# Optimization experiments

Hardware: AMD Instinct MI355X
Metric: run time of the kernel (lower is better)

## Reference

```python
import jax, jax.numpy as jnp
import numpy as np

NUM_CLASSES = 10
P_CUTOFF = 0.95
TEMP = 0.5  # temperature used throughout the original forward
B_LB, B_ULB, D = 4096, 6144, 128


def _l2_normalize(x, eps=1e-12):
    # matches torch.nn.functional.normalize(x, dim=1)
    n = jnp.linalg.norm(x, axis=1, keepdims=True)
    return x / jnp.maximum(n, eps)


def setup_inputs() -> dict:
    key = jax.random.key(0)
    k = jax.random.split(key, 6)
    anchor_feat = jax.random.normal(k[0], (B_ULB, D), jnp.float32)
    positive_feat = jax.random.normal(k[1], (B_ULB, D), jnp.float32)
    lb_feat = jax.random.normal(k[2], (B_LB, D), jnp.float32)
    labels = jax.random.randint(k[3], (B_LB,), 0, NUM_CLASSES)
    lb_one_hot = jax.nn.one_hot(labels, NUM_CLASSES, dtype=jnp.float32)
    # scale logits so a realistic fraction of unlabeled samples pass the 0.95 cutoff
    logits_x_ulb_1 = 3.0 * jax.random.normal(k[4], (B_ULB, NUM_CLASSES), jnp.float32)
    logits_x_ulb_2 = 3.0 * jax.random.normal(k[5], (B_ULB, NUM_CLASSES), jnp.float32)
    return {
        "anchor_feat": anchor_feat,
        "positive_feat": positive_feat,
        "lb_feat": lb_feat,
        "lb_one_hot": lb_one_hot,
        "logits_x_ulb_1": logits_x_ulb_1,
        "logits_x_ulb_2": logits_x_ulb_2,
    }


def reference(anchor_feat, positive_feat, lb_feat, lb_one_hot,
              logits_x_ulb_1, logits_x_ulb_2):
    # pick the more-confident view per unlabeled sample
    prob1 = jax.nn.softmax(logits_x_ulb_1 / TEMP, axis=1)
    prob2 = jax.nn.softmax(logits_x_ulb_2 / TEMP, axis=1)
    take1 = jnp.max(prob1, axis=-1) >= jnp.max(prob2, axis=-1)
    logits_gt = jnp.where(take1[:, None], logits_x_ulb_1, logits_x_ulb_2)

    # confidence mask at p_cutoff = 0.95
    mask = (jax.nn.softmax(logits_gt, axis=1) >= P_CUTOFF).astype(logits_gt.dtype)
    logits_gt = logits_gt * mask

    # per-class counts: labeled via one-hot sum; unlabeled via vectorized bincount
    class_num_lb = lb_one_hot.sum(axis=0)
    max_val = jnp.max(logits_gt, axis=1)
    max_idx = jnp.argmax(logits_gt, axis=1)
    valid = (max_val != 0).astype(jnp.float32)  # max_val==0 -> idx -1 -> skipped
    class_num_ulb = jnp.zeros((NUM_CLASSES,), jnp.float32).at[max_idx].add(valid) * 2.0
    class_num = class_num_ulb + class_num_lb

    # build [B_lb + 2*B_ulb, 10] target distribution
    logits_x_ulb = jnp.concatenate([logits_gt, logits_gt], axis=0)
    prob_xulb = jax.nn.softmax(logits_x_ulb / TEMP, axis=-1)
    logits_bf = jnp.concatenate([lb_one_hot, prob_xulb], axis=0)  # [N, 10]

    # self-attention over normalized features (second normalize in the original
    # is idempotent on already unit-norm rows)
    feats = _l2_normalize(jnp.concatenate([lb_feat, anchor_feat, positive_feat], axis=0))  # [N, D]
    attn = jax.nn.softmax(feats @ feats.T / TEMP, axis=1)  # [N, N]
    self_atten = attn @ logits_bf  # [N, 10]

    # per-class division; zero-count classes divided by total count
    denom = jnp.where(class_num == 0, class_num.sum(), class_num)
    logits_af = self_atten / denom[None, :]
    return logits_af
```

## Files before the change

### kernel.cpp

```cpp
#include <hip/hip_runtime.h>
#include <hip/hip_bf16.h>

#define NLB 4096
#define NULB 6144
#define NROWS 16384
#define DD 128
#define NC 10
#define VW 12
#define SEG 16
#define JSEG (NROWS / SEG)
#define NTILE (JSEG / 64)
#define BI 256
#define BJ 64
#define NVB 256
#define SQRTC 1.6986437f

typedef __bf16 bf16_t;
typedef _Float16 f16_t;
typedef f16_t f16x8 __attribute__((ext_vector_type(8)));
typedef float f32x4 __attribute__((ext_vector_type(4)));
typedef short i16x2 __attribute__((ext_vector_type(2)));
typedef int i32x8 __attribute__((ext_vector_type(8)));
typedef unsigned int u32;
typedef unsigned char u8;

__device__ __forceinline__ size_t f8idx(int row, int c) {
  return ((size_t)(row >> 7) << 14) + (size_t)((row & 127) << 7)
       + (size_t)(((c ^ (row & 7)) & 7) << 4);
}

__device__ __forceinline__ u32 packexp2f16(float c0, float c1) {
#if __has_builtin(__builtin_amdgcn_cvt_pknorm_i16)
  float y0 = fmaf(c0, 1.2207465e-4f, 0.46740490f);
  float y1 = fmaf(c1, 1.2207465e-4f, 0.46740490f);
  union { i16x2 p; u32 u; } cv;
  cv.p = __builtin_amdgcn_cvt_pknorm_i16(y0, y1);
  return cv.u;
#else
  u32 b0 = (u32)(int)fmaf(c0, 4.0f, 15315.354f);
  u32 b1 = (u32)(int)fmaf(c1, 4.0f, 15315.354f);
  return __builtin_amdgcn_perm(b1, b0, 0x05040100u);
#endif
}

__global__ void kprep2(const float* __restrict__ lb, const float* __restrict__ an,
                       const float* __restrict__ po, const float* __restrict__ onehot,
                       const float* __restrict__ l1, const float* __restrict__ l2,
                       u8* __restrict__ F8, f16_t* __restrict__ VF,
                       float* __restrict__ clsPart) {
  __shared__ float Vtmp[64 * 16];
  __shared__ float lcnt[NC];
  int b = blockIdx.x;
  int t = threadIdx.x;

  if (b < 1024) {
    int row = b * 16 + (t >> 4);
    int c = t & 15;
    const float* src;
    if (row < NLB) src = lb + (size_t)row * DD;
    else if (row < NLB + NULB) src = an + (size_t)(row - NLB) * DD;
    else src = po + (size_t)(row - NLB - NULB) * DD;
    float4 v0 = ((const float4*)src)[c * 2];
    float4 v1 = ((const float4*)src)[c * 2 + 1];
    float ss = v0.x*v0.x + v0.y*v0.y + v0.z*v0.z + v0.w*v0.w
             + v1.x*v1.x + v1.y*v1.y + v1.z*v1.z + v1.w*v1.w;
#pragma unroll
    for (int off = 8; off >= 1; off >>= 1) ss += __shfl_xor(ss, off);
    float inv = (16.0f * SQRTC) / fmaxf(sqrtf(ss), 1e-12f);
    u32 d0 = (u32)__builtin_amdgcn_cvt_pk_fp8_f32(v0.x*inv, v0.y*inv, 0, false);
    d0 = (u32)__builtin_amdgcn_cvt_pk_fp8_f32(v0.z*inv, v0.w*inv, d0, true);
    u32 d1 = (u32)__builtin_amdgcn_cvt_pk_fp8_f32(v1.x*inv, v1.y*inv, 0, false);
    d1 = (u32)__builtin_amdgcn_cvt_pk_fp8_f32(v1.z*inv, v1.w*inv, d1, true);
    uint2 dd = {d0, d1};
    *(uint2*)(F8 + f8idx(row, c >> 1) + ((c & 1) << 3)) = dd;
    return;
  }

  int vb = b - 1024;
  if (t < NC) lcnt[t] = 0.0f;
  __syncthreads();
  if (t < 64) {
    int gid = vb * 64 + t;
    float p[16];
    p[10] = 1.0f; p[11] = 0.f; p[12] = 0.f; p[13] = 0.f; p[14] = 0.f; p[15] = 0.f;
    if (gid < NLB) {
      int idx = 0;
#pragma unroll
      for (int c = 0; c < NC; ++c) {
        p[c] = onehot[(size_t)gid * NC + c];
        if (p[c] == 1.0f) idx = c;
      }
      atomicAdd(&lcnt[idx], 1.0f);
    } else {
      int r = (gid < NLB + NULB) ? (gid - NLB) : (gid - NLB - NULB);
      bool count = (gid < NLB + NULB);
      float a[NC], bb[NC];
#pragma unroll
      for (int c = 0; c < NC; ++c) { a[c] = l1[(size_t)r * NC + c]; bb[c] = l2[(size_t)r * NC + c]; }
      float m1 = a[0], m2 = bb[0];
#pragma unroll
      for (int c = 1; c < NC; ++c) { m1 = fmaxf(m1, a[c]); m2 = fmaxf(m2, bb[c]); }
      float s1 = 0.0f, s2 = 0.0f;
#pragma unroll
      for (int c = 0; c < NC; ++c) {
        s1 += expf(2.0f * (a[c] - m1));
        s2 += expf(2.0f * (bb[c] - m2));
      }
      bool take1 = (s1 <= s2);
      float g[NC];
#pragma unroll
      for (int c = 0; c < NC; ++c) g[c] = take1 ? a[c] : bb[c];
      float mg = g[0];
#pragma unroll
      for (int c = 1; c < NC; ++c) mg = fmaxf(mg, g[c]);
      float e[NC]; float sg = 0.0f;
#pragma unroll
      for (int c = 0; c < NC; ++c) { e[c] = expf(g[c] - mg); sg += e[c]; }
      float msk[NC];
#pragma unroll
      for (int c = 0; c < NC; ++c) msk[c] = ((e[c] / sg) >= 0.95f) ? g[c] : 0.0f;
      float mx = msk[0]; int mi = 0;
#pragma unroll
      for (int c = 1; c < NC; ++c) if (msk[c] > mx) { mx = msk[c]; mi = c; }
      if (count && mx != 0.0f) atomicAdd(&lcnt[mi], 2.0f);
      float mm = 2.0f * msk[0];
#pragma unroll
      for (int c = 1; c < NC; ++c) mm = fmaxf(mm, 2.0f * msk[c]);
      float q[NC]; float sp = 0.0f;
#pragma unroll
      for (int c = 0; c < NC; ++c) { q[c] = expf(2.0f * msk[c] - mm); sp += q[c]; }
#pragma unroll
      for (int c = 0; c < NC; ++c) p[c] = q[c] / sp;
    }
#pragma unroll
    for (int c = 0; c < 16; ++c) Vtmp[t * 16 + c] = p[c];
  }
  __syncthreads();
  if (t < 16) clsPart[(size_t)vb * 16 + t] = (t < NC) ? lcnt[t] : 0.0f;
  if (t < 128) {
    int gbase = vb * 2;
    int G = t >> 6;
    int l = t & 63;
    int q = l >> 4;
    int n = l & 15;
    union { f16_t h[8]; uint4 uu; } pk;
#pragma unroll
    for (int d = 0; d < 4; ++d) {
      pk.h[d]     = (f16_t)Vtmp[(G * 32      + q * 4 + d) * 16 + n];
      pk.h[4 + d] = (f16_t)Vtmp[(G * 32 + 16 + q * 4 + d) * 16 + n];
    }
    *(uint4*)(VF + ((size_t)(gbase + G) * 64 + l) * 8) = pk.uu;
  }
}

#define WAITV(n) asm volatile("s_waitcnt vmcnt(" #n ")" ::: "memory")
__launch_bounds__(256, 4)
__global__ void kattn(const u8* __restrict__ F8, const f16_t* __restrict__ VF,
                      float* __restrict__ Ppart) {
  __shared__ __align__(16) u8 Fs[3][BJ * 128];
  __shared__ uint4 Vs4[3][128];
  int t = threadIdx.x;
  int lane = t & 63;
  int wave = t >> 6;
  int q = lane >> 4;
  int r = lane & 15;
  int i0 = blockIdx.x * BI + wave * 64;
  int jbase = blockIdx.y * JSEG;

  i32x8 bfr[4];
#pragma unroll
  for (int s = 0; s < 4; ++s) {
    int row = i0 + s * 16 + r;
    union { uint4 h[2]; i32x8 v; } bb;
    bb.h[0] = *(const uint4*)(F8 + f8idx(row, 2 * q));
    bb.h[1] = *(const uint4*)(F8 + f8idx(row, 2 * q + 1));
    bfr[s] = bb.v;
  }

  f32x4 acc[4];
#pragma unroll
  for (int s = 0; s < 4; ++s) acc[s] = (f32x4){0.f, 0.f, 0.f, 0.f};
  const f32x4 kZero = {0.f, 0.f, 0.f, 0.f};

  auto stage = [&](int buf, int j0) {
    const uint4* srcF = (const uint4*)(F8 + (((size_t)(j0 >> 7)) << 14)
                                          + (((size_t)(j0 & 64)) << 7));
#pragma unroll
    for (int k = 0; k < 2; ++k) {
      int off = (k << 8) + t;
      __builtin_amdgcn_global_load_lds(
          (const __attribute__((address_space(1))) uint4*)(srcF + off),
          (__attribute__((address_space(3))) uint4*)((uint4*)Fs[buf] + off), 16, 0, 0);
    }
    int vc = t & 127;
    const uint4* srcV = (const uint4*)VF + ((size_t)(j0 >> 5) << 6);
    __builtin_amdgcn_global_load_lds(
        (const __attribute__((address_space(1))) uint4*)(srcV + vc),
        (__attribute__((address_space(3))) uint4*)(Vs4[buf] + vc), 16, 0, 0);
  };

  auto compute = [&](int buf) {
    const u8* fsb = Fs[buf];
    const uint4* vsb = Vs4[buf];
#pragma unroll
    for (int jp = 0; jp < 2; ++jp) {
      union { uint4 h[2]; i32x8 v; } afe, afo;
      const u8* re = fsb + (jp * 32 + r) * 128;
      const u8* ro = re + 16 * 128;
      int c0 = (((2 * q) ^ (r & 7)) & 7) << 4;
      int c1 = (((2 * q + 1) ^ (r & 7)) & 7) << 4;
      afe.h[0] = *(const uint4*)(re + c0);
      afe.h[1] = *(const uint4*)(re + c1);
      afo.h[0] = *(const uint4*)(ro + c0);
      afo.h[1] = *(const uint4*)(ro + c1);
      union { uint4 qd; f16x8 v; } bv;
      bv.qd = vsb[jp * 64 + lane];

      __builtin_amdgcn_s_setprio(1);
      f32x4 ce = __builtin_amdgcn_mfma_scale_f32_16x16x128_f8f6f4(
          afe.v, bfr[0], kZero, 0, 0, 0, 0x7F7F7F7Fu, 0, 0x7F7F7F7Fu);
      f32x4 co = __builtin_amdgcn_mfma_scale_f32_16x16x128_f8f6f4(
          afo.v, bfr[0], kZero, 0, 0, 0, 0x7F7F7F7Fu, 0, 0x7F7F7F7Fu);
      __builtin_amdgcn_s_setprio(0);
#pragma unroll
      for (int s = 0; s < 4; ++s) {
        f32x4 cen, con;
        if (s < 3) {
          __builtin_amdgcn_s_setprio(1);
          cen = __builtin_amdgcn_mfma_scale_f32_16x16x128_f8f6f4(
              afe.v, bfr[s + 1], kZero, 0, 0, 0, 0x7F7F7F7Fu, 0, 0x7F7F7F7Fu);
          con = __builtin_amdgcn_mfma_scale_f32_16x16x128_f8f6f4(
              afo.v, bfr[s + 1], kZero, 0, 0, 0, 0x7F7F7F7Fu, 0, 0x7F7F7F7Fu);
          __builtin_amdgcn_s_setprio(0);
        }
        union { u32 u[4]; f16x8 v; } pf;
        pf.u[0] = packexp2f16(ce[0], ce[1]);
        pf.u[1] = packexp2f16(ce[2], ce[3]);
        pf.u[2] = packexp2f16(co[0], co[1]);
        pf.u[3] = packexp2f16(co[2], co[3]);
        __builtin_amdgcn_s_setprio(1);
        acc[s] = __builtin_amdgcn_mfma_f32_16x16x32_f16(pf.v, bv.v, acc[s], 0, 0, 0);
        __builtin_amdgcn_s_setprio(0);
        if (s < 3) { ce = cen; co = con; }
      }
    }
  };

  stage(0, jbase);
  stage(1, jbase + BJ);
#pragma unroll
  for (int jt = 0; jt < NTILE; ++jt) {
    if (jt + 2 < NTILE) stage((jt + 2) % 3, jbase + (jt + 2) * BJ);
    if (jt + 2 < NTILE)      { WAITV(6); }
    else if (jt + 1 < NTILE) { WAITV(3); }
    else                     { WAITV(0); }
    __builtin_amdgcn_s_barrier();
    __builtin_amdgcn_sched_barrier(0);
    compute(jt % 3);
    __builtin_amdgcn_sched_barrier(0);
    __builtin_amdgcn_s_barrier();
  }

  if (r < 12) {
    float* base = Ppart + ((size_t)blockIdx.y * NROWS + (size_t)i0) * VW;
#pragma unroll
    for (int s = 0; s < 4; ++s) {
      float* op = base + (s * 16 + q * 4) * VW + r;
      op[0 * VW] = acc[s][0];
      op[1 * VW] = acc[s][1];
      op[2 * VW] = acc[s][2];
      op[3 * VW] = acc[s][3];
    }
  }
}

__global__ void kfinal(float* __restrict__ out, const float* __restrict__ Ppart,
                       const float* __restrict__ clsPart) {
  __shared__ float clsS[16];
  int t = threadIdx.x;
  const float4* cp = (const float4*)clsPart;
  float4 c0 = {0.f, 0.f, 0.f, 0.f}, c1 = c0;
  float c2x = 0.f, c2y = 0.f;
#pragma unroll
  for (int k = 0; k < 4; ++k) {
    int rr = t + 64 * k;
    float4 x0 = cp[rr * 4], x1 = cp[rr * 4 + 1], x2 = cp[rr * 4 + 2];
    c0.x += x0.x; c0.y += x0.y; c0.z += x0.z; c0.w += x0.w;
    c1.x += x1.x; c1.y += x1.y; c1.z += x1.z; c1.w += x1.w;
    c2x += x2.x; c2y += x2.y;
  }
#pragma unroll
  for (int off = 32; off >= 1; off >>= 1) {
    c0.x += __shfl_xor(c0.x, off); c0.y += __shfl_xor(c0.y, off);
    c0.z += __shfl_xor(c0.z, off); c0.w += __shfl_xor(c0.w, off);
    c1.x += __shfl_xor(c1.x, off); c1.y += __shfl_xor(c1.y, off);
    c1.z += __shfl_xor(c1.z, off); c1.w += __shfl_xor(c1.w, off);
    c2x += __shfl_xor(c2x, off); c2y += __shfl_xor(c2y, off);
  }
  if (t == 0) {
    *(float4*)&clsS[0] = c0;
    *(float4*)&clsS[4] = c1;
    clsS[8] = c2x; clsS[9] = c2y;
    clsS[10] = 0.f; clsS[11] = 0.f; clsS[12] = 0.f;
    clsS[13] = 0.f; clsS[14] = 0.f; clsS[15] = 0.f;
  }
  __syncthreads();
  float d[NC]; float tot = 0.0f;
#pragma unroll
  for (int c = 0; c < NC; ++c) { d[c] = clsS[c]; tot += d[c]; }

  int row = blockIdx.x * 64 + t;
  float4 a0 = {0.f, 0.f, 0.f, 0.f}, a1 = a0, a2 = a0;
#pragma unroll
  for (int s = 0; s < SEG; ++s) {
    const float4* pr = (const float4*)(Ppart + ((size_t)s * NROWS + (size_t)row) * VW);
    float4 x0 = pr[0], x1 = pr[1], x2 = pr[2];
    a0.x += x0.x; a0.y += x0.y; a0.z += x0.z; a0.w += x0.w;
    a1.x += x1.x; a1.y += x1.y; a1.z += x1.z; a1.w += x1.w;
    a2.x += x2.x; a2.y += x2.y; a2.z += x2.z;
  }
  float num[NC] = {a0.x, a0.y, a0.z, a0.w, a1.x, a1.y, a1.z, a1.w, a2.x, a2.y};
  float rs = 1.0f / a2.z;
  float* op = out + (size_t)row * NC;
#pragma unroll
  for (int c = 0; c < NC; ++c) {
    float den = (d[c] == 0.0f) ? tot : d[c];
    op[c] = num[c] * rs / den;
  }
}

extern "C" void kernel_launch(void* const* d_in, const int* in_sizes, int n_in,
                              void* d_out, int out_size, void* d_ws, size_t ws_size,
                              hipStream_t stream) {
  const float* anchor   = (const float*)d_in[0];
  const float* positive = (const float*)d_in[1];
  const float* lbfeat   = (const float*)d_in[2];
  const float* onehot   = (const float*)d_in[3];
  const float* l1       = (const float*)d_in[4];
  const float* l2       = (const float*)d_in[5];
  float* out = (float*)d_out;

  char* ws = (char*)d_ws;
  u8*     F8      = (u8*)ws;
  f16_t*  VF      = (f16_t*)(ws + 2097152);
  float*  Ppart   = (float*)(ws + 2097152 + 524288);
  float*  clsPart = (float*)(ws + 2097152 + 524288 + (size_t)SEG * NROWS * VW * 4);

  kprep2<<<1024 + NVB, 256, 0, stream>>>(lbfeat, anchor, positive, onehot, l1, l2,
                                         F8, VF, clsPart);
  kattn<<<dim3(NROWS / BI, SEG), 256, 0, stream>>>(F8, VF, Ppart);
  kfinal<<<NVB, 64, 0, stream>>>(out, Ppart, clsPart);
}
```

Measured before the change: 112.0 us.

## Fuse prep, attention and final reduce into one cooperative kernel with grid syncs

Merges the three launches into a single cooperative kernel of 1024 blocks that runs the prep, attention and reduction phases separated by grid-wide syncs. Prep now handles 16 value rows per block alongside feature quantization, and the final reduction spreads the 16 segment partials across lanes with shuffles. If the cooperative launch fails it falls back to three separate kernels. The aim is to remove inter-kernel launch gaps and tail effects, at the cost of grid-sync overhead and a fixed 1024-block grid that must be co-resident at 4 blocks per CU.

```diff
diff --git a/kernel.cpp b/kernel.cpp
--- a/kernel.cpp
+++ b/kernel.cpp
@@ -1,5 +1,8 @@
 #include <hip/hip_runtime.h>
 #include <hip/hip_bf16.h>
+#include <hip/hip_cooperative_groups.h>
+
+namespace cg = cooperative_groups;
 
 #define NLB 4096
 #define NULB 6144
@@ -12,7 +15,6 @@
 #define NTILE (JSEG / 64)
 #define BI 256
 #define BJ 64
-#define NVB 256
 #define SQRTC 1.6986437f
 
 typedef __bf16 bf16_t;
@@ -43,17 +45,15 @@
 #endif
 }
 
-__global__ void kprep2(const float* __restrict__ lb, const float* __restrict__ an,
-                       const float* __restrict__ po, const float* __restrict__ onehot,
-                       const float* __restrict__ l1, const float* __restrict__ l2,
-                       u8* __restrict__ F8, f16_t* __restrict__ VF,
-                       float* __restrict__ clsPart) {
-  __shared__ float Vtmp[64 * 16];
-  __shared__ float lcnt[NC];
-  int b = blockIdx.x;
-  int t = threadIdx.x;
-
-  if (b < 1024) {
+__device__ __forceinline__ void phaseA(
+    const float* __restrict__ lb, const float* __restrict__ an,
+    const float* __restrict__ po, const float* __restrict__ onehot,
+    const float* __restrict__ l1, const float* __restrict__ l2,
+    u8* __restrict__ F8, f16_t* __restrict__ VF, float* __restrict__ clsPart,
+    int b, int t) {
+  __shared__ float Vtmp[16 * 16];
+  __shared__ float lcnt[16];
+  {
     int row = b * 16 + (t >> 4);
     int c = t & 15;
     const float* src;
@@ -73,14 +73,11 @@
     d1 = (u32)__builtin_amdgcn_cvt_pk_fp8_f32(v1.z*inv, v1.w*inv, d1, true);
     uint2 dd = {d0, d1};
     *(uint2*)(F8 + f8idx(row, c >> 1) + ((c & 1) << 3)) = dd;
-    return;
-  }
-
-  int vb = b - 1024;
-  if (t < NC) lcnt[t] = 0.0f;
+  }
+  if (t < 16) lcnt[t] = 0.0f;
   __syncthreads();
-  if (t < 64) {
-    int gid = vb * 64 + t;
+  if (t < 16) {
+    int gid = b * 16 + t;
     float p[16];
     p[10] = 1.0f; p[11] = 0.f; p[12] = 0.f; p[13] = 0.f; p[14] = 0.f; p[15] = 0.f;
     if (gid < NLB) {
@@ -136,36 +133,29 @@
     for (int c = 0; c < 16; ++c) Vtmp[t * 16 + c] = p[c];
   }
   __syncthreads();
-  if (t < 16) clsPart[(size_t)vb * 16 + t] = (t < NC) ? lcnt[t] : 0.0f;
-  if (t < 128) {
-    int gbase = vb * 2;
-    int G = t >> 6;
-    int l = t & 63;
-    int q = l >> 4;
-    int n = l & 15;
-    union { f16_t h[8]; uint4 uu; } pk;
-#pragma unroll
-    for (int d = 0; d < 4; ++d) {
-      pk.h[d]     = (f16_t)Vtmp[(G * 32      + q * 4 + d) * 16 + n];
-      pk.h[4 + d] = (f16_t)Vtmp[(G * 32 + 16 + q * 4 + d) * 16 + n];
-    }
-    *(uint4*)(VF + ((size_t)(gbase + G) * 64 + l) * 8) = pk.uu;
+  if (t < 16) clsPart[(size_t)b * 16 + t] = (t < NC) ? lcnt[t] : 0.0f;
+  if (t < 64) {
+    int l = t, q = l >> 4, n = l & 15;
+    union { f16_t h[4]; uint2 u; } pk;
+#pragma unroll
+    for (int d = 0; d < 4; ++d) pk.h[d] = (f16_t)Vtmp[(q * 4 + d) * 16 + n];
+    *(uint2*)(VF + ((size_t)(b >> 1) * 64 + l) * 8 + (size_t)(b & 1) * 4) = pk.u;
   }
 }
 
 #define WAITV(n) asm volatile("s_waitcnt vmcnt(" #n ")" ::: "memory")
-__launch_bounds__(256, 4)
-__global__ void kattn(const u8* __restrict__ F8, const f16_t* __restrict__ VF,
-                      float* __restrict__ Ppart) {
+__device__ __forceinline__ void phaseB(const u8* __restrict__ F8,
+                                       const f16_t* __restrict__ VF,
+                                       float* __restrict__ Ppart,
+                                       int bx, int by, int t) {
   __shared__ __align__(16) u8 Fs[3][BJ * 128];
   __shared__ uint4 Vs4[3][128];
-  int t = threadIdx.x;
   int lane = t & 63;
   int wave = t >> 6;
   int q = lane >> 4;
   int r = lane & 15;
-  int i0 = blockIdx.x * BI + wave * 64;
-  int jbase = blockIdx.y * JSEG;
+  int i0 = bx * BI + wave * 64;
+  int jbase = by * JSEG;
 
   i32x8 bfr[4];
 #pragma unroll
@@ -262,7 +252,7 @@
   }
 
   if (r < 12) {
-    float* base = Ppart + ((size_t)blockIdx.y * NROWS + (size_t)i0) * VW;
+    float* base = Ppart + ((size_t)by * NROWS + (size_t)i0) * VW;
 #pragma unroll
     for (int s = 0; s < 4; ++s) {
       float* op = base + (s * 16 + q * 4) * VW + r;
@@ -274,59 +264,84 @@
   }
 }
 
-__global__ void kfinal(float* __restrict__ out, const float* __restrict__ Ppart,
-                       const float* __restrict__ clsPart) {
+__device__ __forceinline__ void phaseC(float* __restrict__ out,
+                                       const float* __restrict__ Ppart,
+                                       const float* __restrict__ clsPart,
+                                       int b, int t) {
+  __shared__ float4 LDSc[4][4];
   __shared__ float clsS[16];
-  int t = threadIdx.x;
   const float4* cp = (const float4*)clsPart;
-  float4 c0 = {0.f, 0.f, 0.f, 0.f}, c1 = c0;
-  float c2x = 0.f, c2y = 0.f;
-#pragma unroll
-  for (int k = 0; k < 4; ++k) {
-    int rr = t + 64 * k;
-    float4 x0 = cp[rr * 4], x1 = cp[rr * 4 + 1], x2 = cp[rr * 4 + 2];
-    c0.x += x0.x; c0.y += x0.y; c0.z += x0.z; c0.w += x0.w;
-    c1.x += x1.x; c1.y += x1.y; c1.z += x1.z; c1.w += x1.w;
-    c2x += x2.x; c2y += x2.y;
-  }
-#pragma unroll
-  for (int off = 32; off >= 1; off >>= 1) {
-    c0.x += __shfl_xor(c0.x, off); c0.y += __shfl_xor(c0.y, off);
-    c0.z += __shfl_xor(c0.z, off); c0.w += __shfl_xor(c0.w, off);
-    c1.x += __shfl_xor(c1.x, off); c1.y += __shfl_xor(c1.y, off);
-    c1.z += __shfl_xor(c1.z, off); c1.w += __shfl_xor(c1.w, off);
-    c2x += __shfl_xor(c2x, off); c2y += __shfl_xor(c2y, off);
-  }
-  if (t == 0) {
-    *(float4*)&clsS[0] = c0;
-    *(float4*)&clsS[4] = c1;
-    clsS[8] = c2x; clsS[9] = c2y;
-    clsS[10] = 0.f; clsS[11] = 0.f; clsS[12] = 0.f;
-    clsS[13] = 0.f; clsS[14] = 0.f; clsS[15] = 0.f;
-  }
+  float4 ca = {0.f, 0.f, 0.f, 0.f};
+#pragma unroll
+  for (int k = 0; k < 16; ++k) {
+    float4 x = cp[t + 256 * k];
+    ca.x += x.x; ca.y += x.y; ca.z += x.z; ca.w += x.w;
+  }
+#pragma unroll
+  for (int off = 4; off <= 32; off <<= 1) {
+    ca.x += __shfl_xor(ca.x, off); ca.y += __shfl_xor(ca.y, off);
+    ca.z += __shfl_xor(ca.z, off); ca.w += __shfl_xor(ca.w, off);
+  }
+  int wv = t >> 6, ln = t & 63;
+  if (ln < 4) LDSc[wv][ln] = ca;
   __syncthreads();
-  float d[NC]; float tot = 0.0f;
-#pragma unroll
-  for (int c = 0; c < NC; ++c) { d[c] = clsS[c]; tot += d[c]; }
-
-  int row = blockIdx.x * 64 + t;
-  float4 a0 = {0.f, 0.f, 0.f, 0.f}, a1 = a0, a2 = a0;
-#pragma unroll
-  for (int s = 0; s < SEG; ++s) {
-    const float4* pr = (const float4*)(Ppart + ((size_t)s * NROWS + (size_t)row) * VW);
-    float4 x0 = pr[0], x1 = pr[1], x2 = pr[2];
-    a0.x += x0.x; a0.y += x0.y; a0.z += x0.z; a0.w += x0.w;
-    a1.x += x1.x; a1.y += x1.y; a1.z += x1.z; a1.w += x1.w;
-    a2.x += x2.x; a2.y += x2.y; a2.z += x2.z;
-  }
-  float num[NC] = {a0.x, a0.y, a0.z, a0.w, a1.x, a1.y, a1.z, a1.w, a2.x, a2.y};
-  float rs = 1.0f / a2.z;
-  float* op = out + (size_t)row * NC;
-#pragma unroll
-  for (int c = 0; c < NC; ++c) {
-    float den = (d[c] == 0.0f) ? tot : d[c];
-    op[c] = num[c] * rs / den;
-  }
+  if (t < 4) {
+    float4 s0 = LDSc[0][t], s1 = LDSc[1][t], s2 = LDSc[2][t], s3 = LDSc[3][t];
+    float4 s = {s0.x + s1.x + s2.x + s3.x, s0.y + s1.y + s2.y + s3.y,
+                s0.z + s1.z + s2.z + s3.z, s0.w + s1.w + s2.w + s3.w};
+    *(float4*)&clsS[t * 4] = s;
+  }
+  __syncthreads();
+
+  int row = b * 16 + (t >> 4);
+  int s = t & 15;
+  const float4* pr = (const float4*)(Ppart + ((size_t)s * NROWS + (size_t)row) * VW);
+  float4 a0 = pr[0], a1 = pr[1], a2 = pr[2];
+#pragma unroll
+  for (int off = 1; off <= 8; off <<= 1) {
+    a0.x += __shfl_xor(a0.x, off); a0.y += __shfl_xor(a0.y, off);
+    a0.z += __shfl_xor(a0.z, off); a0.w += __shfl_xor(a0.w, off);
+    a1.x += __shfl_xor(a1.x, off); a1.y += __shfl_xor(a1.y, off);
+    a1.z += __shfl_xor(a1.z, off); a1.w += __shfl_xor(a1.w, off);
+    a2.x += __shfl_xor(a2.x, off); a2.y += __shfl_xor(a2.y, off);
+    a2.z += __shfl_xor(a2.z, off);
+  }
+  if (s < NC) {
+    float num = (s == 0) ? a0.x : (s == 1) ? a0.y : (s == 2) ? a0.z : (s == 3) ? a0.w
+              : (s == 4) ? a1.x : (s == 5) ? a1.y : (s == 6) ? a1.z : (s == 7) ? a1.w
+              : (s == 8) ? a2.x : a2.y;
+    float d = clsS[s];
+    float tot = clsS[0] + clsS[1] + clsS[2] + clsS[3] + clsS[4]
+              + clsS[5] + clsS[6] + clsS[7] + clsS[8] + clsS[9];
+    float den = (d == 0.0f) ? tot : d;
+    float rs = 1.0f / a2.z;
+    out[(size_t)row * NC + s] = num * rs / den;
+  }
+}
+
+__launch_bounds__(256, 4)
+__global__ void kfused(const float* lb, const float* an, const float* po,
+                       const float* onehot, const float* l1, const float* l2,
+                       u8* F8, f16_t* VF, float* clsPart, float* Ppart, float* out) {
+  int b = blockIdx.x, t = threadIdx.x;
+  phaseA(lb, an, po, onehot, l1, l2, F8, VF, clsPart, b, t);
+  cg::this_grid().sync();
+  phaseB(F8, VF, Ppart, b & 63, b >> 6, t);
+  cg::this_grid().sync();
+  phaseC(out, Ppart, clsPart, b, t);
+}
+
+__global__ void kA(const float* lb, const float* an, const float* po,
+                   const float* onehot, const float* l1, const float* l2,
+                   u8* F8, f16_t* VF, float* clsPart) {
+  phaseA(lb, an, po, onehot, l1, l2, F8, VF, clsPart, blockIdx.x, threadIdx.x);
+}
+__launch_bounds__(256, 4)
+__global__ void kB(const u8* F8, const f16_t* VF, float* Ppart) {
+  phaseB(F8, VF, Ppart, blockIdx.x, blockIdx.y, threadIdx.x);
+}
+__global__ void kC(float* out, const float* Ppart, const float* clsPart) {
+  phaseC(out, Ppart, clsPart, blockIdx.x, threadIdx.x);
 }
 
 extern "C" void kernel_launch(void* const* d_in, const int* in_sizes, int n_in,
@@ -346,8 +361,15 @@
   float*  Ppart   = (float*)(ws + 2097152 + 524288);
   float*  clsPart = (float*)(ws + 2097152 + 524288 + (size_t)SEG * NROWS * VW * 4);
 
-  kprep2<<<1024 + NVB, 256, 0, stream>>>(lbfeat, anchor, positive, onehot, l1, l2,
-                                         F8, VF, clsPart);
-  kattn<<<dim3(NROWS / BI, SEG), 256, 0, stream>>>(F8, VF, Ppart);
-  kfinal<<<NVB, 64, 0, stream>>>(out, Ppart, clsPart);
-}
+  void* args[] = {(void*)&lbfeat, (void*)&anchor, (void*)&positive, (void*)&onehot,
+                  (void*)&l1, (void*)&l2, (void*)&F8, (void*)&VF,
+                  (void*)&clsPart, (void*)&Ppart, (void*)&out};
+  hipError_t e = hipLaunchCooperativeKernel(reinterpret_cast<void*>(kfused),
+                                            dim3(1024), dim3(256), args, 0, stream);
+  if (e != hipSuccess) {
+    kA<<<1024, 256, 0, stream>>>(lbfeat, anchor, positive, onehot, l1, l2,
+                                 F8, VF, clsPart);
+    kB<<<dim3(64, SEG), 256, 0, stream>>>(F8, VF, Ppart);
+    kC<<<1024, 256, 0, stream>>>(out, Ppart, clsPart);
+  }
+}
```

Measured after the change: 364.0 us. 3.25x slower.
